# Kernel optimization log

Hardware: AMD Instinct MI355X
Metric: run time of the kernel (lower is better)

## Reference

```python
import jax, jax.numpy as jnp
import numpy as np

WS = 10
NUM_HEADS = 12
DIM = 384


def setup_inputs() -> dict:
    key = jax.random.key(0)
    k1, k2, k3 = jax.random.split(key, 3)
    B, t, H, W, C = 2, 4, 44, 44, DIM
    x = jax.random.normal(k1, (B * t, H * W, C), dtype=jnp.float32)
    qkv_w = jax.random.normal(k2, (3 * C, C), dtype=jnp.float32) * 0.02
    proj_w = jax.random.normal(k3, (C, C), dtype=jnp.float32) * 0.02
    proj_b = jnp.zeros((C,), dtype=jnp.float32)
    return {"x": x, "qkv_w": qkv_w, "proj_w": proj_w, "proj_b": proj_b,
            "t": t, "H": H, "W": W}


def reference(x, qkv_w, proj_w, proj_b, t, H, W):
    ws, nh = WS, NUM_HEADS
    BT, N, C = x.shape
    B = BT // t
    hd = C // nh
    scale = hd ** (-0.5)

    ax = x.reshape(B, t, H, W, C)
    pad_r = (ws - W % ws) % ws
    pad_b = (ws - H % ws) % ws
    if pad_r > 0 or pad_b > 0:
        ax = jnp.pad(ax, ((0, 0), (0, 0), (0, pad_b), (0, pad_r), (0, 0)))
    hg, wg = (H + ws - 1) // ws, (W + ws - 1) // ws
    # partition into windows: each window holds t*ws*ws tokens
    ax = ax.reshape(B, t, hg, ws, wg, ws, C)
    ax = ax.transpose(0, 2, 4, 1, 3, 5, 6).reshape(B, hg * wg, t * ws * ws, C)

    qkv = ax @ qkv_w.T  # (B, nw, n, 3C)
    qkv = qkv.reshape(B, hg * wg, t * ws * ws, 3, nh, hd)
    qkv = qkv.transpose(3, 0, 1, 4, 2, 5)  # (3, B, nw, nh, n, hd)
    q, k, v = qkv[0], qkv[1], qkv[2]

    attn = jnp.einsum('bwhnd,bwhmd->bwhnm', q, k) * scale
    attn = jax.nn.softmax(attn, axis=-1)
    out = jnp.einsum('bwhnm,bwhmd->bwhnd', attn, v)  # (B, nw, nh, n, hd)
    out = out.transpose(0, 1, 3, 2, 4).reshape(B, hg * wg, t * ws * ws, C)

    # reverse window partition
    out = out.reshape(B, hg, wg, t, ws, ws, C)
    out = out.transpose(0, 3, 1, 4, 2, 5, 6).reshape(B, t, hg * ws, wg * ws, C)
    out = out[:, :, :H, :W, :]
    out = out.reshape(B, t * H * W, C)
    out = out @ proj_w.T + proj_b
    return out.reshape(-1, N, C)
```

## Files before the change

kernel.cpp:

```cpp
#include <hip/hip_runtime.h>
#include <cstddef>

typedef __attribute__((ext_vector_type(8))) short bf16x8;
typedef __attribute__((ext_vector_type(4))) float f32x4;
typedef __attribute__((ext_vector_type(16))) float f32x16;
typedef unsigned short ushort_t;

namespace {
constexpr int Tt = 4, Hh = 44, Ww = 44, Cc = 384, NH = 12, HD = 32;
constexpr int NWIN = 25, NT = 400, NTP = 416, NPOS = Hh * Ww;
constexpr int NTOK = 2 * Tt * NPOS;
constexpr float SCALE = 0.17677669529663687f;
constexpr float LOG2E = 1.4426950408889634f;
constexpr size_t XN  = (size_t)NTOK * Cc;
constexpr size_t WN  = (size_t)3 * Cc * Cc;
constexpr size_t PWN = (size_t)Cc * Cc;
constexpr size_t PLN = (size_t)600 * NTP * HD;
}

__device__ __forceinline__ ushort_t f2bf(float f) {
  unsigned u = __builtin_bit_cast(unsigned, f);
  u += 0x7fffu + ((u >> 16) & 1u);
  return (ushort_t)(u >> 16);
}

__device__ __forceinline__ unsigned cvt_pk_bf16(float a, float b) {
  unsigned r;
  asm volatile("v_cvt_pk_bf16_f32 %0, %1, %2" : "=v"(r) : "v"(a), "v"(b));
  return r;
}

__device__ __forceinline__ void gload16(const void* g, void* l) {
  __builtin_amdgcn_global_load_lds(
      (const __attribute__((address_space(1))) unsigned int*)g,
      (__attribute__((address_space(3))) unsigned int*)l, 16, 0, 0);
}

__global__ __launch_bounds__(256) void conv_all(
    const float* __restrict__ x, const float* __restrict__ w1,
    const float* __restrict__ w2, ushort_t* __restrict__ xo,
    ushort_t* __restrict__ w1o, ushort_t* __restrict__ w2o,
    ushort_t* __restrict__ qpl, ushort_t* __restrict__ kpl,
    ushort_t* __restrict__ vpl) {
  constexpr int XN8 = (int)(XN / 8), WN8 = (int)(WN / 8), PN8 = (int)(PWN / 8);
  constexpr int TOT8 = XN8 + WN8 + PN8;
  constexpr int ZTOT = 50 * NTP * NH;
  const int i = blockIdx.x * 256 + threadIdx.x;
  if (i < TOT8) {
    const float* s;
    ushort_t* d;
    int j;
    if (i < XN8)            { s = x;  d = xo;  j = i; }
    else if (i < XN8 + WN8) { s = w1; d = w1o; j = i - XN8; }
    else                    { s = w2; d = w2o; j = i - XN8 - WN8; }
    const float4* s4 = (const float4*)s;
    float4 a = s4[2 * j], bq = s4[2 * j + 1];
    union { bf16x8 v; ushort_t u[8]; } o;
    o.u[0] = f2bf(a.x);  o.u[1] = f2bf(a.y);  o.u[2] = f2bf(a.z);  o.u[3] = f2bf(a.w);
    o.u[4] = f2bf(bq.x); o.u[5] = f2bf(bq.y); o.u[6] = f2bf(bq.z); o.u[7] = f2bf(bq.w);
    ((bf16x8*)d)[j] = o.v;
  } else if (i < TOT8 + ZTOT) {
    const int j = i - TOT8;
    const int pair = j / NH, head = j - pair * NH;
    const int bw = pair / NTP, kk = pair - bw * NTP;
    const int win = bw % NWIN, hi5 = win / 5, wi5 = win % 5;
    bool fill;
    if (kk >= NT) {
      fill = true;
    } else {
      const int rem = kk % 100;
      const int hh = rem / 10, ww2 = rem - hh * 10;
      fill = (hi5 == 4 && hh >= 4) || (wi5 == 4 && ww2 >= 4);
    }
    if (fill) {
      const size_t off = ((size_t)(bw * NH + head) * NTP + kk) * HD;
      bf16x8 z;
      z[0]=0;z[1]=0;z[2]=0;z[3]=0;z[4]=0;z[5]=0;z[6]=0;z[7]=0;
#pragma unroll
      for (int p = 0; p < 4; ++p) {
        ((bf16x8*)(qpl + off))[p] = z;
        ((bf16x8*)(kpl + off))[p] = z;
        ((bf16x8*)(vpl + off))[p] = z;
      }
    }
  }
}

__global__ __launch_bounds__(256) void qkv_mfma(
    const ushort_t* __restrict__ xb, const ushort_t* __restrict__ wb,
    ushort_t* __restrict__ qpl, ushort_t* __restrict__ kpl,
    ushort_t* __restrict__ vpl) {
  __shared__ __align__(16) unsigned char As[8192];
  __shared__ __align__(16) unsigned char Bs[8192];
  const unsigned bid = blockIdx.x;
  const unsigned xcd = bid & 7u, slot = bid >> 3;
  const unsigned wgid = (xcd == 0 ? 0u : 137u + (xcd - 1u) * 136u) + slot;
  const int nt = wgid % 9, mt = wgid / 9;
  const int tid = threadIdx.x, lane = tid & 63, wid = tid >> 6;
  const int wm = wid >> 1, wn = wid & 1;
  const int g = lane >> 4, q = lane & 15;
  const int m0 = mt * 128, n0 = nt * 128;

  const unsigned char* xB = (const unsigned char*)xb;
  const unsigned char* wB = (const unsigned char*)wb;

  size_t aoff[2], boff[2];
  unsigned ldsoff[2];
#pragma unroll
  for (int p = 0; p < 2; ++p) {
    const int row = wid * 32 + p * 16 + (lane >> 2);
    const int gs = (lane & 3) ^ ((row >> 1) & 3);
    aoff[p] = (size_t)(m0 + row) * 768 + gs * 16;
    boff[p] = (size_t)(n0 + row) * 768 + gs * 16;
    ldsoff[p] = wid * 2048 + p * 1024;
  }

  f32x4 acc[4][4] = {};

  for (int kb = 0; kb < 12; ++kb) {
    if (kb) __syncthreads();
#pragma unroll
    for (int p = 0; p < 2; ++p) {
      gload16(xB + aoff[p] + kb * 64, As + ldsoff[p]);
      gload16(wB + boff[p] + kb * 64, Bs + ldsoff[p]);
    }
    __syncthreads();
    bf16x8 tfr[4], wfr[4];
#pragma unroll
    for (int i = 0; i < 4; ++i) {
      const int ar = wm * 64 + i * 16 + q;
      tfr[i] = *(const bf16x8*)(As + ar * 64 + ((g ^ ((ar >> 1) & 3)) << 4));
      const int br = wn * 64 + i * 16 + q;
      wfr[i] = *(const bf16x8*)(Bs + br * 64 + ((g ^ ((br >> 1) & 3)) << 4));
    }
#pragma unroll
    for (int i = 0; i < 4; ++i)
#pragma unroll
      for (int j = 0; j < 4; ++j)
        acc[i][j] = __builtin_amdgcn_mfma_f32_16x16x32_bf16(wfr[i], tfr[j],
                                                            acc[i][j], 0, 0, 0);
  }

  const float QS = SCALE * LOG2E;
#pragma unroll
  for (int j = 0; j < 4; ++j) {
    const int t = m0 + wm * 64 + j * 16 + q;
    const int bt = t / NPOS, pos = t - bt * NPOS;
    const int h = pos / Ww, w = pos - h * Ww;
    const int b = bt >> 2, tt = bt & 3;
    const int hq = h / 10, wq = w / 10;
    const int kk = tt * 100 + (h - hq * 10) * 10 + (w - wq * 10);
    const int bw = b * NWIN + hq * 5 + wq;
#pragma unroll
    for (int i = 0; i < 4; ++i) {
      const int col = n0 + wn * 64 + i * 16 + 4 * g;
      const int which = col / Cc;
      const int head = (col - which * Cc) >> 5;
      const int d4 = col & 31;
      ushort_t* pl = which == 0 ? qpl : (which == 1 ? kpl : vpl);
      const float scl = which == 0 ? QS : 1.0f;
      uint2 st;
      st.x = cvt_pk_bf16(acc[i][j][0] * scl, acc[i][j][1] * scl);
      st.y = cvt_pk_bf16(acc[i][j][2] * scl, acc[i][j][3] * scl);
      *(uint2*)(pl + ((size_t)(bw * NH + head) * NTP + kk) * HD + d4) = st;
    }
  }
}

__global__ __launch_bounds__(832) void attn_mfma(
    const ushort_t* __restrict__ qpl, const ushort_t* __restrict__ kpl,
    const ushort_t* __restrict__ vpl, ushort_t* __restrict__ aout) {
  __shared__ __align__(16) unsigned char Vt[32 * 896];

  const int wh = blockIdx.x;
  const int head = wh % NH, bw = wh / NH;
  const int b = bw / NWIN, win = bw % NWIN, hi5 = win / 5, wi5 = win % 5;

  const int tid = threadIdx.x, lane = tid & 63, wid = tid >> 6;
  const int l31 = lane & 31, hi = lane >> 5;

  const ushort_t* qbase = qpl + (size_t)wh * (NTP * HD);
  const ushort_t* kbase = kpl + (size_t)wh * (NTP * HD);
  const ushort_t* vbase = vpl + (size_t)wh * (NTP * HD);

  const int qrow = wid * 32 + l31;
  const ushort_t* qp = qbase + (size_t)qrow * HD;
  const bf16x8 qfa = *(const bf16x8*)(qp + hi * 8);
  const bf16x8 qfb = *(const bf16x8*)(qp + 16 + hi * 8);

  unsigned koff = (unsigned)l31 * HD;
  bf16x8 kf0 = *(const bf16x8*)(kbase + koff + hi * 8);
  bf16x8 kf1 = *(const bf16x8*)(kbase + koff + 16 + hi * 8);

  for (int slot = tid; slot < 1664; slot += 832) {
    const int key = slot >> 2, dblk = (slot & 3) * 8;
    union { bf16x8 v; ushort_t u[8]; } t;
    t.v = *(const bf16x8*)(vbase + (size_t)key * HD + dblk);
    const int kc = key >> 3, klo = key & 7;
#pragma unroll
    for (int j = 0; j < 8; ++j) {
      const int d = dblk + j;
      const int f = (d & 7) ^ ((d >> 3) & 3);
      *(ushort_t*)(Vt + d * 896 + ((kc ^ f) << 4) + klo * 2) = t.u[j];
    }
  }
  __syncthreads();

  const int fv = (l31 & 7) ^ ((l31 >> 3) & 3);
  const unsigned char* vrow = Vt + l31 * 896;

  f32x16 o = {};
  float lpart = 0.f;

  for (int c = 0; c < 13; ++c) {
    f32x16 s = {};
    __builtin_amdgcn_s_setprio(1);
    s = __builtin_amdgcn_mfma_f32_32x32x16_bf16(kf0, qfa, s, 0, 0, 0);
    s = __builtin_amdgcn_mfma_f32_32x32x16_bf16(kf1, qfb, s, 0, 0, 0);
    __builtin_amdgcn_s_setprio(0);

    if (c < 12) {
      koff += 32u * HD;
      kf0 = *(const bf16x8*)(kbase + koff + hi * 8);
      kf1 = *(const bf16x8*)(kbase + koff + 16 + hi * 8);
    }

    if (c == 12) {
#pragma unroll
      for (int r = 8; r < 16; ++r) s[r] = -1e30f;
    }

    float e[16];
#pragma unroll
    for (int r = 0; r < 16; ++r) e[r] = __builtin_amdgcn_exp2f(s[r]);
    lpart += ((e[0] + e[1]) + (e[2] + e[3])) + ((e[4] + e[5]) + (e[6] + e[7])) +
             (((e[8] + e[9]) + (e[10] + e[11])) +
              ((e[12] + e[13]) + (e[14] + e[15])));

    unsigned w0 = cvt_pk_bf16(e[0], e[1]),   w1 = cvt_pk_bf16(e[2], e[3]);
    unsigned w2 = cvt_pk_bf16(e[4], e[5]),   w3 = cvt_pk_bf16(e[6], e[7]);
    unsigned w4 = cvt_pk_bf16(e[8], e[9]),   w5 = cvt_pk_bf16(e[10], e[11]);
    unsigned w6 = cvt_pk_bf16(e[12], e[13]), w7 = cvt_pk_bf16(e[14], e[15]);
    asm volatile("v_permlane32_swap_b32 %0, %1" : "+v"(w0), "+v"(w2));
    asm volatile("v_permlane32_swap_b32 %0, %1" : "+v"(w1), "+v"(w3));
    asm volatile("v_permlane32_swap_b32 %0, %1" : "+v"(w4), "+v"(w6));
    asm volatile("v_permlane32_swap_b32 %0, %1" : "+v"(w5), "+v"(w7));
    union { bf16x8 v; unsigned u[4]; } p0, p1;
    p0.u[0] = w0; p0.u[1] = w1; p0.u[2] = w2; p0.u[3] = w3;
    p1.u[0] = w4; p1.u[1] = w5; p1.u[2] = w6; p1.u[3] = w7;

    const bf16x8 vf0 = *(const bf16x8*)(vrow + (((4 * c + hi) ^ fv) << 4));
    const bf16x8 vf1 = *(const bf16x8*)(vrow + (((4 * c + 2 + hi) ^ fv) << 4));
    __builtin_amdgcn_s_setprio(1);
    o = __builtin_amdgcn_mfma_f32_32x32x16_bf16(vf0, p0.v, o, 0, 0, 0);
    o = __builtin_amdgcn_mfma_f32_32x32x16_bf16(vf1, p1.v, o, 0, 0, 0);
    __builtin_amdgcn_s_setprio(0);
  }

  lpart += __shfl_xor(lpart, 32);

  {
    const int tt = qrow / 100, rem = qrow - tt * 100;
    const int hh = rem / 10, ww2 = rem - hh * 10;
    const int h = hi5 * 10 + hh, w = wi5 * 10 + ww2;
    if (qrow < NT && h < Hh && w < Ww) {
      const int qtok = (b * Tt + tt) * NPOS + h * Ww + w;
      ushort_t* dst = aout + (size_t)qtok * Cc + head * HD;
      const float inv = 1.0f / lpart;
#pragma unroll
      for (int g4 = 0; g4 < 4; ++g4) {
        unsigned lo  = cvt_pk_bf16(o[4 * g4 + 0] * inv, o[4 * g4 + 1] * inv);
        unsigned hi2 = cvt_pk_bf16(o[4 * g4 + 2] * inv, o[4 * g4 + 3] * inv);
        uint2 st; st.x = lo; st.y = hi2;
        *(uint2*)(dst + 8 * g4 + 4 * hi) = st;
      }
    }
  }
}

__global__ __launch_bounds__(256) void proj_mfma(
    const ushort_t* __restrict__ ab, const ushort_t* __restrict__ pw,
    const float* __restrict__ bias, float* __restrict__ out) {
  __shared__ __align__(16) unsigned char As[8192];
  __shared__ __align__(16) unsigned char Bs[8192];
  const int nt = blockIdx.x, mt = blockIdx.y;
  const int tid = threadIdx.x, lane = tid & 63, wid = tid >> 6;
  const int wm = wid >> 1, wn = wid & 1;
  const int g = lane >> 4, q = lane & 15;
  const int m0 = mt * 128, n0 = nt * 128;

  const unsigned char* aB = (const unsigned char*)ab;
  const unsigned char* wB = (const unsigned char*)pw;

  size_t aoff[2], boff[2];
  unsigned ldsoff[2];
#pragma unroll
  for (int p = 0; p < 2; ++p) {
    const int row = wid * 32 + p * 16 + (lane >> 2);
    const int gs = (lane & 3) ^ ((row >> 1) & 3);
    aoff[p] = (size_t)(m0 + row) * 768 + gs * 16;
    boff[p] = (size_t)(n0 + row) * 768 + gs * 16;
    ldsoff[p] = wid * 2048 + p * 1024;
  }

  f32x4 acc[4][4] = {};

  for (int kb = 0; kb < 12; ++kb) {
    if (kb) __syncthreads();
#pragma unroll
    for (int p = 0; p < 2; ++p) {
      gload16(aB + aoff[p] + kb * 64, As + ldsoff[p]);
      gload16(wB + boff[p] + kb * 64, Bs + ldsoff[p]);
    }
    __syncthreads();
    bf16x8 tfr[4], wfr[4];
#pragma unroll
    for (int i = 0; i < 4; ++i) {
      const int ar = wm * 64 + i * 16 + q;
      tfr[i] = *(const bf16x8*)(As + ar * 64 + ((g ^ ((ar >> 1) & 3)) << 4));
      const int br = wn * 64 + i * 16 + q;
      wfr[i] = *(const bf16x8*)(Bs + br * 64 + ((g ^ ((br >> 1) & 3)) << 4));
    }
#pragma unroll
    for (int i = 0; i < 4; ++i)
#pragma unroll
      for (int j = 0; j < 4; ++j)
        acc[i][j] = __builtin_amdgcn_mfma_f32_16x16x32_bf16(wfr[i], tfr[j],
                                                            acc[i][j], 0, 0, 0);
  }

#pragma unroll
  for (int j = 0; j < 4; ++j) {
    const int t = m0 + wm * 64 + j * 16 + q;
#pragma unroll
    for (int i = 0; i < 4; ++i) {
      const int col = n0 + wn * 64 + i * 16 + 4 * g;
      const float4 bb = *(const float4*)(bias + col);
      float4 st;
      st.x = acc[i][j][0] + bb.x;
      st.y = acc[i][j][1] + bb.y;
      st.z = acc[i][j][2] + bb.z;
      st.w = acc[i][j][3] + bb.w;
      *(float4*)(out + (size_t)t * Cc + col) = st;
    }
  }
}

extern "C" void kernel_launch(void* const* d_in, const int* in_sizes, int n_in,
                              void* d_out, int out_size, void* d_ws,
                              size_t ws_size, hipStream_t stream) {
  const float* x      = (const float*)d_in[0];
  const float* qkv_w  = (const float*)d_in[1];
  const float* proj_w = (const float*)d_in[2];
  const float* proj_b = (const float*)d_in[3];

  ushort_t* xb    = (ushort_t*)d_ws;
  ushort_t* wb    = xb + XN;
  ushort_t* pwb   = wb + WN;
  ushort_t* qpl   = pwb + PWN;
  ushort_t* kpl   = qpl + PLN;
  ushort_t* vpl   = kpl + PLN;
  ushort_t* attnb = vpl + PLN;

  constexpr int TOT8 = (int)((XN + WN + PWN) / 8);
  constexpr int ZTOT = 50 * NTP * NH;
  conv_all<<<(TOT8 + ZTOT + 255) / 256, 256, 0, stream>>>(
      x, qkv_w, proj_w, xb, wb, pwb, qpl, kpl, vpl);
  qkv_mfma<<<1089, 256, 0, stream>>>(xb, wb, qpl, kpl, vpl);
  attn_mfma<<<600, 832, 0, stream>>>(qpl, kpl, vpl, attnb);
  proj_mfma<<<dim3(3, 121), 256, 0, stream>>>(attnb, pwb, proj_b, (float*)d_out);
}
```

Measured before the change: 89.40 us.

## Store Q in token-major layout and loop attention tiles over fewer waves

Q is now written in natural token-major layout from the QKV GEMM instead of the padded per-window plane, so zero-filling of the Q plane is dropped and the Q epilogue skips the window index math. The attention kernel drops from 13 waves to 7 per block, each wave looping over query tiles and gathering Q rows directly from token positions. This cuts zero-fill traffic and raises per-block occupancy flexibility, but Q loads become strided gathers and waves doing two tiles lengthen the critical path.

Measured after the change: 90.56 us. About the same (+1.3%).

```diff
diff --git a/kernel.cpp b/kernel.cpp
--- a/kernel.cpp
+++ b/kernel.cpp
@@ -40,8 +40,7 @@
     const float* __restrict__ x, const float* __restrict__ w1,
     const float* __restrict__ w2, ushort_t* __restrict__ xo,
     ushort_t* __restrict__ w1o, ushort_t* __restrict__ w2o,
-    ushort_t* __restrict__ qpl, ushort_t* __restrict__ kpl,
-    ushort_t* __restrict__ vpl) {
+    ushort_t* __restrict__ kpl, ushort_t* __restrict__ vpl) {
   constexpr int XN8 = (int)(XN / 8), WN8 = (int)(WN / 8), PN8 = (int)(PWN / 8);
   constexpr int TOT8 = XN8 + WN8 + PN8;
   constexpr int ZTOT = 50 * NTP * NH;
@@ -78,7 +77,6 @@
       z[0]=0;z[1]=0;z[2]=0;z[3]=0;z[4]=0;z[5]=0;z[6]=0;z[7]=0;
 #pragma unroll
       for (int p = 0; p < 4; ++p) {
-        ((bf16x8*)(qpl + off))[p] = z;
         ((bf16x8*)(kpl + off))[p] = z;
         ((bf16x8*)(vpl + off))[p] = z;
       }
@@ -88,7 +86,7 @@
 
 __global__ __launch_bounds__(256) void qkv_mfma(
     const ushort_t* __restrict__ xb, const ushort_t* __restrict__ wb,
-    ushort_t* __restrict__ qpl, ushort_t* __restrict__ kpl,
+    ushort_t* __restrict__ qd, ushort_t* __restrict__ kpl,
     ushort_t* __restrict__ vpl) {
   __shared__ __align__(16) unsigned char As[8192];
   __shared__ __align__(16) unsigned char Bs[8192];
@@ -141,34 +139,49 @@
                                                             acc[i][j], 0, 0, 0);
   }
 
-  const float QS = SCALE * LOG2E;
-#pragma unroll
-  for (int j = 0; j < 4; ++j) {
-    const int t = m0 + wm * 64 + j * 16 + q;
-    const int bt = t / NPOS, pos = t - bt * NPOS;
-    const int h = pos / Ww, w = pos - h * Ww;
-    const int b = bt >> 2, tt = bt & 3;
-    const int hq = h / 10, wq = w / 10;
-    const int kk = tt * 100 + (h - hq * 10) * 10 + (w - wq * 10);
-    const int bw = b * NWIN + hq * 5 + wq;
-#pragma unroll
-    for (int i = 0; i < 4; ++i) {
-      const int col = n0 + wn * 64 + i * 16 + 4 * g;
-      const int which = col / Cc;
-      const int head = (col - which * Cc) >> 5;
-      const int d4 = col & 31;
-      ushort_t* pl = which == 0 ? qpl : (which == 1 ? kpl : vpl);
-      const float scl = which == 0 ? QS : 1.0f;
-      uint2 st;
-      st.x = cvt_pk_bf16(acc[i][j][0] * scl, acc[i][j][1] * scl);
-      st.y = cvt_pk_bf16(acc[i][j][2] * scl, acc[i][j][3] * scl);
-      *(uint2*)(pl + ((size_t)(bw * NH + head) * NTP + kk) * HD + d4) = st;
-    }
-  }
-}
-
-__global__ __launch_bounds__(832) void attn_mfma(
-    const ushort_t* __restrict__ qpl, const ushort_t* __restrict__ kpl,
+  if (nt < 3) {
+    const float QS = SCALE * LOG2E;
+#pragma unroll
+    for (int j = 0; j < 4; ++j) {
+      const int t = m0 + wm * 64 + j * 16 + q;
+      ushort_t* dst = qd + (size_t)t * Cc;
+#pragma unroll
+      for (int i = 0; i < 4; ++i) {
+        const int col = n0 + wn * 64 + i * 16 + 4 * g;
+        uint2 st;
+        st.x = cvt_pk_bf16(acc[i][j][0] * QS, acc[i][j][1] * QS);
+        st.y = cvt_pk_bf16(acc[i][j][2] * QS, acc[i][j][3] * QS);
+        *(uint2*)(dst + col) = st;
+      }
+    }
+  } else {
+    const int which = nt / 3;
+    ushort_t* pl = (which == 1) ? kpl : vpl;
+#pragma unroll
+    for (int j = 0; j < 4; ++j) {
+      const int t = m0 + wm * 64 + j * 16 + q;
+      const int bt = t / NPOS, pos = t - bt * NPOS;
+      const int h = pos / Ww, w = pos - h * Ww;
+      const int b = bt >> 2, tt = bt & 3;
+      const int hq = h / 10, wq = w / 10;
+      const int kk = tt * 100 + (h - hq * 10) * 10 + (w - wq * 10);
+      const int bw = b * NWIN + hq * 5 + wq;
+#pragma unroll
+      for (int i = 0; i < 4; ++i) {
+        const int col = n0 + wn * 64 + i * 16 + 4 * g;
+        const int head = (col - which * Cc) >> 5;
+        const int d4 = col & 31;
+        uint2 st;
+        st.x = cvt_pk_bf16(acc[i][j][0], acc[i][j][1]);
+        st.y = cvt_pk_bf16(acc[i][j][2], acc[i][j][3]);
+        *(uint2*)(pl + ((size_t)(bw * NH + head) * NTP + kk) * HD + d4) = st;
+      }
+    }
+  }
+}
+
+__global__ __launch_bounds__(448) void attn_mfma(
+    const ushort_t* __restrict__ qd, const ushort_t* __restrict__ kpl,
     const ushort_t* __restrict__ vpl, ushort_t* __restrict__ aout) {
   __shared__ __align__(16) unsigned char Vt[32 * 896];
 
@@ -179,20 +192,10 @@
   const int tid = threadIdx.x, lane = tid & 63, wid = tid >> 6;
   const int l31 = lane & 31, hi = lane >> 5;
 
-  const ushort_t* qbase = qpl + (size_t)wh * (NTP * HD);
   const ushort_t* kbase = kpl + (size_t)wh * (NTP * HD);
   const ushort_t* vbase = vpl + (size_t)wh * (NTP * HD);
 
-  const int qrow = wid * 32 + l31;
-  const ushort_t* qp = qbase + (size_t)qrow * HD;
-  const bf16x8 qfa = *(const bf16x8*)(qp + hi * 8);
-  const bf16x8 qfb = *(const bf16x8*)(qp + 16 + hi * 8);
-
-  unsigned koff = (unsigned)l31 * HD;
-  bf16x8 kf0 = *(const bf16x8*)(kbase + koff + hi * 8);
-  bf16x8 kf1 = *(const bf16x8*)(kbase + koff + 16 + hi * 8);
-
-  for (int slot = tid; slot < 1664; slot += 832) {
+  for (int slot = tid; slot < 1664; slot += 448) {
     const int key = slot >> 2, dblk = (slot & 3) * 8;
     union { bf16x8 v; ushort_t u[8]; } t;
     t.v = *(const bf16x8*)(vbase + (size_t)key * HD + dblk);
@@ -209,62 +212,73 @@
   const int fv = (l31 & 7) ^ ((l31 >> 3) & 3);
   const unsigned char* vrow = Vt + l31 * 896;
 
-  f32x16 o = {};
-  float lpart = 0.f;
-
-  for (int c = 0; c < 13; ++c) {
-    f32x16 s = {};
-    __builtin_amdgcn_s_setprio(1);
-    s = __builtin_amdgcn_mfma_f32_32x32x16_bf16(kf0, qfa, s, 0, 0, 0);
-    s = __builtin_amdgcn_mfma_f32_32x32x16_bf16(kf1, qfb, s, 0, 0, 0);
-    __builtin_amdgcn_s_setprio(0);
-
-    if (c < 12) {
-      koff += 32u * HD;
-      kf0 = *(const bf16x8*)(kbase + koff + hi * 8);
-      kf1 = *(const bf16x8*)(kbase + koff + 16 + hi * 8);
-    }
-
-    if (c == 12) {
-#pragma unroll
-      for (int r = 8; r < 16; ++r) s[r] = -1e30f;
-    }
-
-    float e[16];
-#pragma unroll
-    for (int r = 0; r < 16; ++r) e[r] = __builtin_amdgcn_exp2f(s[r]);
-    lpart += ((e[0] + e[1]) + (e[2] + e[3])) + ((e[4] + e[5]) + (e[6] + e[7])) +
-             (((e[8] + e[9]) + (e[10] + e[11])) +
-              ((e[12] + e[13]) + (e[14] + e[15])));
-
-    unsigned w0 = cvt_pk_bf16(e[0], e[1]),   w1 = cvt_pk_bf16(e[2], e[3]);
-    unsigned w2 = cvt_pk_bf16(e[4], e[5]),   w3 = cvt_pk_bf16(e[6], e[7]);
-    unsigned w4 = cvt_pk_bf16(e[8], e[9]),   w5 = cvt_pk_bf16(e[10], e[11]);
-    unsigned w6 = cvt_pk_bf16(e[12], e[13]), w7 = cvt_pk_bf16(e[14], e[15]);
-    asm volatile("v_permlane32_swap_b32 %0, %1" : "+v"(w0), "+v"(w2));
-    asm volatile("v_permlane32_swap_b32 %0, %1" : "+v"(w1), "+v"(w3));
-    asm volatile("v_permlane32_swap_b32 %0, %1" : "+v"(w4), "+v"(w6));
-    asm volatile("v_permlane32_swap_b32 %0, %1" : "+v"(w5), "+v"(w7));
-    union { bf16x8 v; unsigned u[4]; } p0, p1;
-    p0.u[0] = w0; p0.u[1] = w1; p0.u[2] = w2; p0.u[3] = w3;
-    p1.u[0] = w4; p1.u[1] = w5; p1.u[2] = w6; p1.u[3] = w7;
-
-    const bf16x8 vf0 = *(const bf16x8*)(vrow + (((4 * c + hi) ^ fv) << 4));
-    const bf16x8 vf1 = *(const bf16x8*)(vrow + (((4 * c + 2 + hi) ^ fv) << 4));
-    __builtin_amdgcn_s_setprio(1);
-    o = __builtin_amdgcn_mfma_f32_32x32x16_bf16(vf0, p0.v, o, 0, 0, 0);
-    o = __builtin_amdgcn_mfma_f32_32x32x16_bf16(vf1, p1.v, o, 0, 0, 0);
-    __builtin_amdgcn_s_setprio(0);
-  }
-
-  lpart += __shfl_xor(lpart, 32);
-
-  {
+  for (int tile = wid; tile < 13; tile += 7) {
+    const int qrow = tile * 32 + l31;
     const int tt = qrow / 100, rem = qrow - tt * 100;
     const int hh = rem / 10, ww2 = rem - hh * 10;
     const int h = hi5 * 10 + hh, w = wi5 * 10 + ww2;
-    if (qrow < NT && h < Hh && w < Ww) {
-      const int qtok = (b * Tt + tt) * NPOS + h * Ww + w;
+    const bool qv = (qrow < NT) && (h < Hh) && (w < Ww);
+    const int qtok = qv ? (b * Tt + tt) * NPOS + h * Ww + w : 0;
+
+    const ushort_t* qp = qd + (size_t)qtok * Cc + head * HD;
+    const bf16x8 qfa = *(const bf16x8*)(qp + hi * 8);
+    const bf16x8 qfb = *(const bf16x8*)(qp + 16 + hi * 8);
+
+    unsigned koff = (unsigned)l31 * HD;
+    bf16x8 kf0 = *(const bf16x8*)(kbase + koff + hi * 8);
+    bf16x8 kf1 = *(const bf16x8*)(kbase + koff + 16 + hi * 8);
+
+    f32x16 o = {};
+    float lpart = 0.f;
+
+    for (int c = 0; c < 13; ++c) {
+      f32x16 s = {};
+      __builtin_amdgcn_s_setprio(1);
+      s = __builtin_amdgcn_mfma_f32_32x32x16_bf16(kf0, qfa, s, 0, 0, 0);
+      s = __builtin_amdgcn_mfma_f32_32x32x16_bf16(kf1, qfb, s, 0, 0, 0);
+      __builtin_amdgcn_s_setprio(0);
+
+      if (c < 12) {
+        koff += 32u * HD;
+        kf0 = *(const bf16x8*)(kbase + koff + hi * 8);
+        kf1 = *(const bf16x8*)(kbase + koff + 16 + hi * 8);
+      }
+
+      if (c == 12) {
+#pragma unroll
+        for (int r = 8; r < 16; ++r) s[r] = -1e30f;
+      }
+
+      float e[16];
+#pragma unroll
+      for (int r = 0; r < 16; ++r) e[r] = __builtin_amdgcn_exp2f(s[r]);
+      lpart += ((e[0] + e[1]) + (e[2] + e[3])) + ((e[4] + e[5]) + (e[6] + e[7])) +
+               (((e[8] + e[9]) + (e[10] + e[11])) +
+                ((e[12] + e[13]) + (e[14] + e[15])));
+
+      unsigned w0 = cvt_pk_bf16(e[0], e[1]),   w1 = cvt_pk_bf16(e[2], e[3]);
+      unsigned w2 = cvt_pk_bf16(e[4], e[5]),   w3 = cvt_pk_bf16(e[6], e[7]);
+      unsigned w4 = cvt_pk_bf16(e[8], e[9]),   w5 = cvt_pk_bf16(e[10], e[11]);
+      unsigned w6 = cvt_pk_bf16(e[12], e[13]), w7 = cvt_pk_bf16(e[14], e[15]);
+      asm volatile("v_permlane32_swap_b32 %0, %1" : "+v"(w0), "+v"(w2));
+      asm volatile("v_permlane32_swap_b32 %0, %1" : "+v"(w1), "+v"(w3));
+      asm volatile("v_permlane32_swap_b32 %0, %1" : "+v"(w4), "+v"(w6));
+      asm volatile("v_permlane32_swap_b32 %0, %1" : "+v"(w5), "+v"(w7));
+      union { bf16x8 v; unsigned u[4]; } p0, p1;
+      p0.u[0] = w0; p0.u[1] = w1; p0.u[2] = w2; p0.u[3] = w3;
+      p1.u[0] = w4; p1.u[1] = w5; p1.u[2] = w6; p1.u[3] = w7;
+
+      const bf16x8 vf0 = *(const bf16x8*)(vrow + (((4 * c + hi) ^ fv) << 4));
+      const bf16x8 vf1 = *(const bf16x8*)(vrow + (((4 * c + 2 + hi) ^ fv) << 4));
+      __builtin_amdgcn_s_setprio(1);
+      o = __builtin_amdgcn_mfma_f32_32x32x16_bf16(vf0, p0.v, o, 0, 0, 0);
+      o = __builtin_amdgcn_mfma_f32_32x32x16_bf16(vf1, p1.v, o, 0, 0, 0);
+      __builtin_amdgcn_s_setprio(0);
+    }
+
+    lpart += __shfl_xor(lpart, 32);
+
+    if (qv) {
       ushort_t* dst = aout + (size_t)qtok * Cc + head * HD;
       const float inv = 1.0f / lpart;
 #pragma unroll
@@ -357,16 +371,16 @@
   ushort_t* xb    = (ushort_t*)d_ws;
   ushort_t* wb    = xb + XN;
   ushort_t* pwb   = wb + WN;
-  ushort_t* qpl   = pwb + PWN;
-  ushort_t* kpl   = qpl + PLN;
+  ushort_t* qd    = pwb + PWN;
+  ushort_t* kpl   = qd + XN;
   ushort_t* vpl   = kpl + PLN;
   ushort_t* attnb = vpl + PLN;
 
   constexpr int TOT8 = (int)((XN + WN + PWN) / 8);
   constexpr int ZTOT = 50 * NTP * NH;
   conv_all<<<(TOT8 + ZTOT + 255) / 256, 256, 0, stream>>>(
-      x, qkv_w, proj_w, xb, wb, pwb, qpl, kpl, vpl);
-  qkv_mfma<<<1089, 256, 0, stream>>>(xb, wb, qpl, kpl, vpl);
-  attn_mfma<<<600, 832, 0, stream>>>(qpl, kpl, vpl, attnb);
+      x, qkv_w, proj_w, xb, wb, pwb, kpl, vpl);
+  qkv_mfma<<<1089, 256, 0, stream>>>(xb, wb, qd, kpl, vpl);
+  attn_mfma<<<600, 448, 0, stream>>>(qd, kpl, vpl, attnb);
   proj_mfma<<<dim3(3, 121), 256, 0, stream>>>(attnb, pwb, proj_b, (float*)d_out);
 }
```
